# Kernel optimization log

Measured on AMD Instinct MI355X. Metric: run time of the kernel, lower is better.

Reference implementation:

```python
import jax, jax.numpy as jnp
import numpy as np

B, L, C, D = 32, 256, 16, 128
WORD_VOCAB, CHR_VOCAB = 50000, 128


def conv1d(x, w, b):
    # x: [N, D, T], w: [D_out, D_in, 3], torch Conv1d (cross-correlation), padding=1
    y = jax.lax.conv_general_dilated(x, w, window_strides=(1,), padding=[(1, 1)],
                                     dimension_numbers=('NCH', 'OIH', 'NCH'))
    return y + b[None, :, None]


def setup_inputs() -> dict:
    key = jax.random.key(0)
    k1, k2, k3, k4, k5, k6, k7, k8 = jax.random.split(key, 8)
    word_vector = jax.random.randint(k1, (B, L), 0, WORD_VOCAB)
    words_in_char = jax.random.randint(k2, (B, L, C), 0, CHR_VOCAB)
    # embedding tables, padding_idx=0 -> row 0 is zeros
    word_table = (jax.random.normal(k3, (WORD_VOCAB, D), jnp.float32) * 0.02).at[0].set(0.0)
    chr_table = (jax.random.normal(k4, (CHR_VOCAB, D), jnp.float32) * 0.02).at[0].set(0.0)
    scale = 1.0 / np.sqrt(D * 3)
    conv_chr_w = jax.random.normal(k5, (D, D, 3), jnp.float32) * scale
    conv_chr_b = jax.random.normal(k6, (D,), jnp.float32) * scale
    conv_word_w = jax.random.normal(k7, (D, D, 3), jnp.float32) * scale
    conv_word_b = jax.random.normal(k8, (D,), jnp.float32) * scale
    return dict(word_vector=word_vector, words_in_char=words_in_char,
                word_table=word_table, chr_table=chr_table,
                conv_chr_w=conv_chr_w, conv_chr_b=conv_chr_b,
                conv_word_w=conv_word_w, conv_word_b=conv_word_b)


def reference(word_vector, words_in_char, word_table, chr_table,
              conv_chr_w, conv_chr_b, conv_word_w, conv_word_b):
    # --- char path (batched version of the per-word Python loop) ---
    chr_emb = chr_table[words_in_char]                       # [B, L, C, D]
    x = chr_emb.reshape(B * L, C, D).transpose(0, 2, 1)      # [B*L, D, C]
    word_conv = conv1d(x, conv_chr_w, conv_chr_b)            # [B*L, D, C]
    char_feats = word_conv.max(axis=2).reshape(B, L, D)      # max over char positions
    # --- word path ---
    word_emb = word_table[word_vector]                       # [B, L, D]
    out = conv1d(word_emb.transpose(0, 2, 1), conv_word_w, conv_word_b)  # [B, D, L]
    # stack both branch outputs into one array: [2, B, D, L]
    return jnp.stack([out, char_feats.transpose(0, 2, 1)])
```

## Files before the change

kernel.cpp:

```cpp
#include <hip/hip_runtime.h>

typedef __attribute__((ext_vector_type(8))) short short8;
typedef __attribute__((ext_vector_type(2))) float float2_t;
typedef __attribute__((ext_vector_type(4))) float float4_t;
typedef __attribute__((ext_vector_type(16))) float float16_t;

#define NB 32
#define NL 256
#define ND 128
#define OUT_PLANE (NB * ND * NL)
#define XS 136
#define BUFSZ (18 * XS)
#define FR_WORD 49152
#define CHRB 98304

__device__ inline unsigned short f2bf(float f) {
    union { float f; unsigned int i; } c;
    c.f = f;
    unsigned int r = c.i + 0x7FFFu + ((c.i >> 16) & 1u);
    return (unsigned short)(r >> 16);
}

__global__ void make_frags(const float* __restrict__ Wc,
                           const float* __restrict__ Ww,
                           const float* __restrict__ chrT,
                           unsigned short* __restrict__ out) {
    const int i0 = (blockIdx.x * 256 + threadIdx.x) * 8;
    unsigned short v[8];
    if (i0 < FR_WORD) {
        int lane = (i0 >> 3) & 63;
        int nt   = (i0 >> 9) & 3;
        int s    = i0 >> 11;
        int dout = nt * 32 + (lane & 31);
        int kk0  = s * 16 + ((lane >> 5) & 1) * 8;
        int t    = kk0 >> 7;
        int d0   = kk0 & 127;
        const float* src = Wc + (dout * 128 + d0) * 3 + t;
#pragma unroll
        for (int j = 0; j < 8; ++j) v[j] = f2bf(src[j * 3]);
    } else if (i0 < CHRB) {
        int ii   = i0 - FR_WORD;
        int lane = (ii >> 3) & 63;
        int nt   = (ii >> 9) & 7;
        int s    = ii >> 12;
        int dout = nt * 16 + (lane & 15);
        int t    = s >> 2;
        int k0   = (s & 3) * 32 + ((lane >> 4) & 3) * 8;
        const float* src = Ww + (dout * 128 + k0) * 3 + t;
#pragma unroll
        for (int j = 0; j < 8; ++j) v[j] = f2bf(src[j * 3]);
    } else {
        const float* src = chrT + (i0 - CHRB);
        float4_t f0 = *(const float4_t*)(src);
        float4_t f1 = *(const float4_t*)(src + 4);
        v[0] = f2bf(f0.x); v[1] = f2bf(f0.y); v[2] = f2bf(f0.z); v[3] = f2bf(f0.w);
        v[4] = f2bf(f1.x); v[5] = f2bf(f1.y); v[6] = f2bf(f1.z); v[7] = f2bf(f1.w);
    }
    *(short8*)&out[i0] = *(const short8*)v;
}

__global__ __launch_bounds__(128, 2) void conv_kernel(
    const int* __restrict__ wv, const int* __restrict__ wic,
    const float* __restrict__ wordT,
    const unsigned short* __restrict__ ws,
    const float* __restrict__ biasC, const float* __restrict__ biasW,
    float* __restrict__ out) {
    __shared__ unsigned short X[4][BUFSZ];
    __shared__ float OT[8][128];
    const int tid  = threadIdx.x;
    const int wave = tid >> 6, lane = tid & 63;
    const int bid = blockIdx.x;

    if (bid < 1024) {
        const unsigned short* chrB = ws + CHRB;
        const int w0 = bid * 8;
        const int b = w0 >> 8, l0 = w0 & 255;
        const int n32 = lane & 31;
        const int h   = (lane >> 5) & 1;
        const int r15 = lane & 15;
        const int wsel = (lane >> 4) & 1;

        short8 bfrag[24][2];
#pragma unroll
        for (int s = 0; s < 24; ++s)
#pragma unroll
            for (int p = 0; p < 2; ++p)
                bfrag[s][p] = *(const short8*)(
                    ws + (((s * 4 + wave * 2 + p) * 64 + lane) << 3));
        float bc[2];
#pragma unroll
        for (int p = 0; p < 2; ++p) bc[p] = biasC[wave * 64 + p * 32 + n32];

        for (int p = tid; p < XS; p += 128)
#pragma unroll
            for (int q = 0; q < 4; ++q) { X[q][p] = 0; X[q][17 * XS + p] = 0; }

        const int ra = tid >> 4, sub = tid & 15;

#pragma unroll
        for (int q = 0; q < 2; ++q) {
            int j0 = wic[(w0 + q) * 16 + ra];
            int j1 = wic[(w0 + q) * 16 + ra + 8];
            short8 g0 = *(const short8*)(chrB + j0 * 128 + sub * 8);
            short8 g1 = *(const short8*)(chrB + j1 * 128 + sub * 8);
            *(short8*)&X[q][(ra + 1) * XS + sub * 8] = g0;
            *(short8*)&X[q][(ra + 9) * XS + sub * 8] = g1;
        }
        int iA0 = wic[(w0 + 2) * 16 + ra];
        int iA1 = wic[(w0 + 2) * 16 + ra + 8];
        int iC0 = wic[(w0 + 3) * 16 + ra];
        int iC1 = wic[(w0 + 3) * 16 + ra + 8];
        __syncthreads();

#pragma unroll
        for (int j = 0; j < 8; j += 2) {
            const unsigned short* abuf = X[(j + wsel) & 3];

            short8 g0, g1;
            if (j < 6) {
                g0 = *(const short8*)(chrB + iA0 * 128 + sub * 8);
                g1 = *(const short8*)(chrB + iA1 * 128 + sub * 8);
            }

            float16_t acc[2];
#pragma unroll
            for (int p = 0; p < 2; ++p)
#pragma unroll
                for (int e = 0; e < 16; ++e) acc[p][e] = 0.f;

#pragma unroll
            for (int s = 0; s < 12; ++s) {
                short8 a = *(const short8*)&abuf[(r15 + (s >> 3)) * XS +
                                                 (s & 7) * 16 + h * 8];
#pragma unroll
                for (int p = 0; p < 2; ++p)
                    acc[p] = __builtin_amdgcn_mfma_f32_32x32x16_bf16(
                        a, bfrag[s][p], acc[p], 0, 0, 0);
            }

            short8 h0, h1;
            if (j < 6) {
                *(short8*)&X[(j + 2) & 3][(ra + 1) * XS + sub * 8] = g0;
                *(short8*)&X[(j + 2) & 3][(ra + 9) * XS + sub * 8] = g1;
                h0 = *(const short8*)(chrB + iC0 * 128 + sub * 8);
                h1 = *(const short8*)(chrB + iC1 * 128 + sub * 8);
                if (j < 4) {
                    iA0 = wic[(w0 + j + 4) * 16 + ra];
                    iA1 = wic[(w0 + j + 4) * 16 + ra + 8];
                    iC0 = wic[(w0 + j + 5) * 16 + ra];
                    iC1 = wic[(w0 + j + 5) * 16 + ra + 8];
                }
            }

#pragma unroll
            for (int s = 12; s < 24; ++s) {
                short8 a = *(const short8*)&abuf[(r15 + (s >> 3)) * XS +
                                                 (s & 7) * 16 + h * 8];
#pragma unroll
                for (int p = 0; p < 2; ++p)
                    acc[p] = __builtin_amdgcn_mfma_f32_32x32x16_bf16(
                        a, bfrag[s][p], acc[p], 0, 0, 0);
            }

            if (j < 6) {
                *(short8*)&X[(j + 3) & 3][(ra + 1) * XS + sub * 8] = h0;
                *(short8*)&X[(j + 3) & 3][(ra + 9) * XS + sub * 8] = h1;
            }

#pragma unroll
            for (int p = 0; p < 2; ++p) {
                float v0 = acc[p][0], v1 = acc[p][8];
#pragma unroll
                for (int e = 1; e < 8; ++e) {
                    v0 = fmaxf(v0, acc[p][e]);
                    v1 = fmaxf(v1, acc[p][e + 8]);
                }
                v0 = fmaxf(v0, __shfl_xor(v0, 32, 64));
                v1 = fmaxf(v1, __shfl_xor(v1, 32, 64));
                if (lane < 32) {
                    int dout = wave * 64 + p * 32 + n32;
                    OT[j][dout]     = v0 + bc[p];
                    OT[j + 1][dout] = v1 + bc[p];
                }
            }
            __syncthreads();
        }

        {
            float r[8];
#pragma unroll
            for (int e = 0; e < 8; ++e) r[e] = OT[e][tid];
            float* obase = out + OUT_PLANE + b * (ND * NL) + tid * NL + l0;
            float4_t s0 = {r[0], r[1], r[2], r[3]};
            float4_t s1 = {r[4], r[5], r[6], r[7]};
            *(float4_t*)&obase[0] = s0;
            *(float4_t*)&obase[4] = s1;
        }
    } else {
        const int wb = bid - 1024;
        const int m = lane & 15, quad = lane >> 4;
        const int b = wb >> 4, l0 = (wb & 15) << 4;
        short8 bfrag[12][4];
#pragma unroll
        for (int s = 0; s < 12; ++s)
#pragma unroll
            for (int p = 0; p < 4; ++p)
                bfrag[s][p] = *(const short8*)(
                    ws + FR_WORD + (((s * 8 + wave * 4 + p) * 64 + lane) << 3));
        float bb[4];
#pragma unroll
        for (int p = 0; p < 4; ++p) bb[p] = biasW[wave * 64 + p * 16 + m];

#pragma unroll
        for (int i0 = 0; i0 < 2; ++i0) {
            int i = tid + i0 * 128;
            if (i < 144) {
                int rr = i >> 3, sg = i & 7;
                int l = l0 + rr - 1;
                int idx = (l >= 0 && l < NL) ? wv[b * NL + l] : 0;
                const float4_t* src =
                    (const float4_t*)(wordT + idx * 128 + sg * 16);
                float4_t f0 = src[0], f1 = src[1], f2 = src[2], f3 = src[3];
                unsigned short t16[16];
                t16[0]=f2bf(f0.x); t16[1]=f2bf(f0.y); t16[2]=f2bf(f0.z); t16[3]=f2bf(f0.w);
                t16[4]=f2bf(f1.x); t16[5]=f2bf(f1.y); t16[6]=f2bf(f1.z); t16[7]=f2bf(f1.w);
                t16[8]=f2bf(f2.x); t16[9]=f2bf(f2.y); t16[10]=f2bf(f2.z); t16[11]=f2bf(f2.w);
                t16[12]=f2bf(f3.x); t16[13]=f2bf(f3.y); t16[14]=f2bf(f3.z); t16[15]=f2bf(f3.w);
                *(short8*)&X[0][rr * XS + sg * 16]     = *(const short8*)&t16[0];
                *(short8*)&X[0][rr * XS + sg * 16 + 8] = *(const short8*)&t16[8];
            }
        }
        __syncthreads();

        float4_t acc[4];
#pragma unroll
        for (int p = 0; p < 4; ++p) acc[p] = (float4_t){0.f, 0.f, 0.f, 0.f};
#pragma unroll
        for (int s = 0; s < 12; ++s) {
            short8 a = *(const short8*)&X[0][(m + (s >> 2)) * XS +
                                            (s & 3) * 32 + quad * 8];
#pragma unroll
            for (int p = 0; p < 4; ++p)
                acc[p] = __builtin_amdgcn_mfma_f32_16x16x32_bf16(
                    a, bfrag[s][p], acc[p], 0, 0, 0);
        }

        float* obase = out + b * (ND * NL) + l0 + quad * 4;
#pragma unroll
        for (int p = 0; p < 4; ++p) {
            int dout = wave * 64 + p * 16 + m;
            float4_t pk;
            pk.x = acc[p].x + bb[p];
            pk.y = acc[p].y + bb[p];
            pk.z = acc[p].z + bb[p];
            pk.w = acc[p].w + bb[p];
            *(float4_t*)&obase[dout * NL] = pk;
        }
    }
}

extern "C" void kernel_launch(void* const* d_in, const int* in_sizes, int n_in,
                              void* d_out, int out_size, void* d_ws,
                              size_t ws_size, hipStream_t stream) {
    const int* word_vector   = (const int*)d_in[0];
    const int* words_in_char = (const int*)d_in[1];
    const float* word_table  = (const float*)d_in[2];
    const float* chr_table   = (const float*)d_in[3];
    const float* conv_chr_w  = (const float*)d_in[4];
    const float* conv_chr_b  = (const float*)d_in[5];
    const float* conv_word_w = (const float*)d_in[6];
    const float* conv_word_b = (const float*)d_in[7];
    float* out            = (float*)d_out;
    unsigned short* wsp   = (unsigned short*)d_ws;

    make_frags<<<56, 256, 0, stream>>>(conv_chr_w, conv_word_w, chr_table, wsp);
    conv_kernel<<<1536, 128, 0, stream>>>(word_vector, words_in_char,
                                          word_table, wsp,
                                          conv_chr_b, conv_word_b, out);
}
```

Before: 102.3 us.

## Stream weight fragments from global per step and process four words per pass

The char-path blocks no longer hold all 48 weight fragments in registers. They reload the B fragments from the workspace on each K step. This frees registers so occupancy can rise to 3 blocks per SIMD via launch_bounds, and the MFMA loop now computes four words at once with four accumulators, reusing each loaded B fragment across two A tiles. The gather pipeline becomes a two-phase prefetch of all eight words, and make_frags moves to smaller blocks. The tradeoff is repeated global/L2 traffic for weights in exchange for more waves, fewer syncs and fewer per-pair iterations.

```diff
diff --git a/kernel.cpp b/kernel.cpp
--- a/kernel.cpp
+++ b/kernel.cpp
@@ -25,7 +25,7 @@
                            const float* __restrict__ Ww,
                            const float* __restrict__ chrT,
                            unsigned short* __restrict__ out) {
-    const int i0 = (blockIdx.x * 256 + threadIdx.x) * 8;
+    const int i0 = (blockIdx.x * 64 + threadIdx.x) * 8;
     unsigned short v[8];
     if (i0 < FR_WORD) {
         int lane = (i0 >> 3) & 63;
@@ -59,7 +59,7 @@
     *(short8*)&out[i0] = *(const short8*)v;
 }
 
-__global__ __launch_bounds__(128, 2) void conv_kernel(
+__global__ __launch_bounds__(128, 3) void conv_kernel(
     const int* __restrict__ wv, const int* __restrict__ wic,
     const float* __restrict__ wordT,
     const unsigned short* __restrict__ ws,
@@ -80,13 +80,6 @@
         const int r15 = lane & 15;
         const int wsel = (lane >> 4) & 1;
 
-        short8 bfrag[24][2];
-#pragma unroll
-        for (int s = 0; s < 24; ++s)
-#pragma unroll
-            for (int p = 0; p < 2; ++p)
-                bfrag[s][p] = *(const short8*)(
-                    ws + (((s * 4 + wave * 2 + p) * 64 + lane) << 3));
         float bc[2];
 #pragma unroll
         for (int p = 0; p < 2; ++p) bc[p] = biasC[wave * 64 + p * 32 + n32];
@@ -97,90 +90,86 @@
 
         const int ra = tid >> 4, sub = tid & 15;
 
-#pragma unroll
-        for (int q = 0; q < 2; ++q) {
-            int j0 = wic[(w0 + q) * 16 + ra];
-            int j1 = wic[(w0 + q) * 16 + ra + 8];
-            short8 g0 = *(const short8*)(chrB + j0 * 128 + sub * 8);
-            short8 g1 = *(const short8*)(chrB + j1 * 128 + sub * 8);
-            *(short8*)&X[q][(ra + 1) * XS + sub * 8] = g0;
-            *(short8*)&X[q][(ra + 9) * XS + sub * 8] = g1;
-        }
-        int iA0 = wic[(w0 + 2) * 16 + ra];
-        int iA1 = wic[(w0 + 2) * 16 + ra + 8];
-        int iC0 = wic[(w0 + 3) * 16 + ra];
-        int iC1 = wic[(w0 + 3) * 16 + ra + 8];
+        int idx0[8], idx1[8];
+#pragma unroll
+        for (int w = 0; w < 8; ++w) {
+            idx0[w] = wic[(w0 + w) * 16 + ra];
+            idx1[w] = wic[(w0 + w) * 16 + ra + 8];
+        }
+
+#pragma unroll
+        for (int w = 0; w < 4; ++w) {
+            short8 g0 = *(const short8*)(chrB + idx0[w] * 128 + sub * 8);
+            short8 g1 = *(const short8*)(chrB + idx1[w] * 128 + sub * 8);
+            *(short8*)&X[w][(ra + 1) * XS + sub * 8] = g0;
+            *(short8*)&X[w][(ra + 9) * XS + sub * 8] = g1;
+        }
         __syncthreads();
 
 #pragma unroll
-        for (int j = 0; j < 8; j += 2) {
-            const unsigned short* abuf = X[(j + wsel) & 3];
-
-            short8 g0, g1;
-            if (j < 6) {
-                g0 = *(const short8*)(chrB + iA0 * 128 + sub * 8);
-                g1 = *(const short8*)(chrB + iA1 * 128 + sub * 8);
-            }
-
-            float16_t acc[2];
-#pragma unroll
-            for (int p = 0; p < 2; ++p)
-#pragma unroll
-                for (int e = 0; e < 16; ++e) acc[p][e] = 0.f;
-
-#pragma unroll
-            for (int s = 0; s < 12; ++s) {
-                short8 a = *(const short8*)&abuf[(r15 + (s >> 3)) * XS +
-                                                 (s & 7) * 16 + h * 8];
-#pragma unroll
-                for (int p = 0; p < 2; ++p)
-                    acc[p] = __builtin_amdgcn_mfma_f32_32x32x16_bf16(
-                        a, bfrag[s][p], acc[p], 0, 0, 0);
-            }
-
-            short8 h0, h1;
-            if (j < 6) {
-                *(short8*)&X[(j + 2) & 3][(ra + 1) * XS + sub * 8] = g0;
-                *(short8*)&X[(j + 2) & 3][(ra + 9) * XS + sub * 8] = g1;
-                h0 = *(const short8*)(chrB + iC0 * 128 + sub * 8);
-                h1 = *(const short8*)(chrB + iC1 * 128 + sub * 8);
-                if (j < 4) {
-                    iA0 = wic[(w0 + j + 4) * 16 + ra];
-                    iA1 = wic[(w0 + j + 4) * 16 + ra + 8];
-                    iC0 = wic[(w0 + j + 5) * 16 + ra];
-                    iC1 = wic[(w0 + j + 5) * 16 + ra + 8];
+        for (int mega = 0; mega < 2; ++mega) {
+            short8 pf[8];
+            if (mega == 0) {
+#pragma unroll
+                for (int w = 0; w < 4; ++w) {
+                    pf[w * 2]     = *(const short8*)(chrB + idx0[4 + w] * 128 +
+                                                     sub * 8);
+                    pf[w * 2 + 1] = *(const short8*)(chrB + idx1[4 + w] * 128 +
+                                                     sub * 8);
                 }
             }
 
-#pragma unroll
-            for (int s = 12; s < 24; ++s) {
-                short8 a = *(const short8*)&abuf[(r15 + (s >> 3)) * XS +
-                                                 (s & 7) * 16 + h * 8];
-#pragma unroll
-                for (int p = 0; p < 2; ++p)
-                    acc[p] = __builtin_amdgcn_mfma_f32_32x32x16_bf16(
-                        a, bfrag[s][p], acc[p], 0, 0, 0);
-            }
-
-            if (j < 6) {
-                *(short8*)&X[(j + 3) & 3][(ra + 1) * XS + sub * 8] = h0;
-                *(short8*)&X[(j + 3) & 3][(ra + 9) * XS + sub * 8] = h1;
-            }
-
-#pragma unroll
-            for (int p = 0; p < 2; ++p) {
-                float v0 = acc[p][0], v1 = acc[p][8];
-#pragma unroll
-                for (int e = 1; e < 8; ++e) {
-                    v0 = fmaxf(v0, acc[p][e]);
-                    v1 = fmaxf(v1, acc[p][e + 8]);
+            float16_t a00, a01, a10, a11;
+#pragma unroll
+            for (int e = 0; e < 16; ++e) {
+                a00[e] = 0.f; a01[e] = 0.f; a10[e] = 0.f; a11[e] = 0.f;
+            }
+
+#pragma unroll 8
+            for (int s = 0; s < 24; ++s) {
+                short8 b0 = *(const short8*)(
+                    ws + (((s * 4 + wave * 2 + 0) * 64 + lane) << 3));
+                short8 b1 = *(const short8*)(
+                    ws + (((s * 4 + wave * 2 + 1) * 64 + lane) << 3));
+                const int aoff = (r15 + (s >> 3)) * XS + (s & 7) * 16 + h * 8;
+                short8 f0 = *(const short8*)&X[wsel][aoff];
+                short8 f1 = *(const short8*)&X[2 + wsel][aoff];
+                a00 = __builtin_amdgcn_mfma_f32_32x32x16_bf16(f0, b0, a00, 0, 0, 0);
+                a01 = __builtin_amdgcn_mfma_f32_32x32x16_bf16(f0, b1, a01, 0, 0, 0);
+                a10 = __builtin_amdgcn_mfma_f32_32x32x16_bf16(f1, b0, a10, 0, 0, 0);
+                a11 = __builtin_amdgcn_mfma_f32_32x32x16_bf16(f1, b1, a11, 0, 0, 0);
+            }
+            __syncthreads();
+
+            if (mega == 0) {
+#pragma unroll
+                for (int w = 0; w < 4; ++w) {
+                    *(short8*)&X[w][(ra + 1) * XS + sub * 8] = pf[w * 2];
+                    *(short8*)&X[w][(ra + 9) * XS + sub * 8] = pf[w * 2 + 1];
                 }
-                v0 = fmaxf(v0, __shfl_xor(v0, 32, 64));
-                v1 = fmaxf(v1, __shfl_xor(v1, 32, 64));
-                if (lane < 32) {
-                    int dout = wave * 64 + p * 32 + n32;
-                    OT[j][dout]     = v0 + bc[p];
-                    OT[j + 1][dout] = v1 + bc[p];
+            }
+
+#pragma unroll
+            for (int pr = 0; pr < 2; ++pr) {
+                const float16_t& ac0 = pr ? a10 : a00;
+                const float16_t& ac1 = pr ? a11 : a01;
+#pragma unroll
+                for (int p = 0; p < 2; ++p) {
+                    const float16_t& ac = p ? ac1 : ac0;
+                    float v0 = ac[0], v1 = ac[8];
+#pragma unroll
+                    for (int e = 1; e < 8; ++e) {
+                        v0 = fmaxf(v0, ac[e]);
+                        v1 = fmaxf(v1, ac[e + 8]);
+                    }
+                    v0 = fmaxf(v0, __shfl_xor(v0, 32, 64));
+                    v1 = fmaxf(v1, __shfl_xor(v1, 32, 64));
+                    if (lane < 32) {
+                        int dout = wave * 64 + p * 32 + n32;
+                        int row = mega * 4 + pr * 2;
+                        OT[row][dout]     = v0 + bc[p];
+                        OT[row + 1][dout] = v1 + bc[p];
+                    }
                 }
             }
             __syncthreads();
@@ -273,7 +262,7 @@
     float* out            = (float*)d_out;
     unsigned short* wsp   = (unsigned short*)d_ws;
 
-    make_frags<<<56, 256, 0, stream>>>(conv_chr_w, conv_word_w, chr_table, wsp);
+    make_frags<<<224, 64, 0, stream>>>(conv_chr_w, conv_word_w, chr_table, wsp);
     conv_kernel<<<1536, 128, 0, stream>>>(word_vector, words_in_char,
                                           word_table, wsp,
                                           conv_chr_b, conv_word_b, out);
```

After: 111.3 us. 1.09x slower.
